# Kernel optimization log

Hardware: AMD Instinct MI355X
Metric: run time of the kernel (lower is better)

The kernel has to match this reference:

```python
import jax, jax.numpy as jnp
import numpy as np

BN_EPS = 1e-5


def setup_inputs() -> dict:
    key = jax.random.key(0)
    ks = jax.random.split(key, 6)
    B, C, N = 8, 256, 2048
    C4 = C // 4
    return {
        "x": jax.random.normal(ks[0], (B, C, N), dtype=jnp.float32),
        "wq": jax.random.normal(ks[1], (C4, C), dtype=jnp.float32) * (1.0 / np.sqrt(C)),
        "wv": jax.random.normal(ks[2], (C, C), dtype=jnp.float32) * (1.0 / np.sqrt(C)),
        "bv": jax.random.normal(ks[3], (C,), dtype=jnp.float32) * 0.02,
        "wt": jax.random.normal(ks[4], (C, C), dtype=jnp.float32) * (1.0 / np.sqrt(C)),
        "bt": jax.random.normal(ks[5], (C,), dtype=jnp.float32) * 0.02,
        "gamma": jnp.ones((C,), dtype=jnp.float32),
        "beta": jnp.zeros((C,), dtype=jnp.float32),
    }


def reference(x, wq, wv, bv, wt, bt, gamma, beta):
    # x: [B, C, N]. Conv1d(kernel=1) == per-point matmul.
    # q_conv and k_conv share the same weight in the original, so q == k.
    q = jnp.einsum('oc,bcn->bon', wq, x)            # [B, C/4, N]
    # ||q_i - q_j||_2 via the Gram identity (same math as norm of the diff tensor)
    sq = jnp.sum(q * q, axis=1)                     # [B, N]
    gram = jnp.einsum('bci,bcj->bij', q, q)         # [B, N, N]
    d2 = sq[:, :, None] - 2.0 * gram + sq[:, None, :]
    l2 = jnp.sqrt(jnp.maximum(d2, 0.0))             # [B, N, N]
    attn = jax.nn.softmax(-l2, axis=-1)             # rows = queries i
    v = jnp.einsum('oc,bcn->bon', wv, x) + bv[None, :, None]   # [B, C, N]
    # einsum('bij,bkj->bik') then permute(0,2,1) == contract j directly to [B, C, N]
    x_r = jnp.einsum('bij,bcj->bci', attn, v)       # [B, C, N]
    t = jnp.einsum('oc,bcn->bon', wt, x_r) + bt[None, :, None]
    # BatchNorm1d in training mode: batch stats over (B, N), biased variance
    mean = jnp.mean(t, axis=(0, 2), keepdims=True)
    var = jnp.mean((t - mean) ** 2, axis=(0, 2), keepdims=True)
    bn = gamma[None, :, None] * (t - mean) * jax.lax.rsqrt(var + BN_EPS) + beta[None, :, None]
    return x + jnp.maximum(bn, 0.0)
```

## Files before the change

kernel.cpp:

```cpp
#include <hip/hip_runtime.h>
#include <math.h>

#define BDIM 8
#define CDIM 256
#define C4DIM 64
#define NDIM 2048
#define LOG2E_SQ 2.0813689810056077f
#define NEG_2LOG2E_SQ -4.1627379620112154f

typedef short bf16x8 __attribute__((ext_vector_type(8)));
typedef float f32x4 __attribute__((ext_vector_type(4)));

__device__ inline unsigned cvt_pk(float lo, float hi) {
  unsigned r;
  asm("v_cvt_pk_bf16_f32 %0, %1, %2" : "=v"(r) : "v"(lo), "v"(hi));
  return r;
}
__device__ inline float bflo(unsigned u) {
  u <<= 16; float f; __builtin_memcpy(&f, &u, 4); return f;
}
__device__ inline float bfhi(unsigned u) {
  u &= 0xffff0000u; float f; __builtin_memcpy(&f, &u, 4); return f;
}

__global__ __launch_bounds__(256) void prep_kernel(const float* __restrict__ x,
                                                   const float* __restrict__ wq,
                                                   const float* __restrict__ wv,
                                                   const float* __restrict__ wt,
                                                   short* __restrict__ xT,
                                                   short* __restrict__ wqb,
                                                   short* __restrict__ wvb,
                                                   short* __restrict__ wtb,
                                                   float* __restrict__ bnsum) {
  __shared__ float tile[64][65];
  const int fb = blockIdx.x, t = threadIdx.x;
  if (fb < 1024) {
    const int b = fb >> 7, c0 = ((fb >> 5) & 3) * 64, n0 = (fb & 31) * 64;
    const int cl = t >> 2, ng = (t & 3) * 16;
#pragma unroll
    for (int kk = 0; kk < 4; ++kk) {
      float4 v = *(const float4*)&x[((size_t)(b * CDIM + c0 + cl)) * NDIM + n0 + ng + kk * 4];
      tile[cl][ng + kk * 4 + 0] = v.x; tile[cl][ng + kk * 4 + 1] = v.y;
      tile[cl][ng + kk * 4 + 2] = v.z; tile[cl][ng + kk * 4 + 3] = v.w;
    }
    __syncthreads();
    const int nl = t >> 2, cg = (t & 3) * 16;
    unsigned u[8];
#pragma unroll
    for (int e = 0; e < 8; ++e)
      u[e] = cvt_pk(tile[cg + 2 * e][nl], tile[cg + 2 * e + 1][nl]);
    short* dst = &xT[((size_t)b * NDIM + n0 + nl) * CDIM + c0 + cg];
    *(uint4*)&dst[0] = make_uint4(u[0], u[1], u[2], u[3]);
    *(uint4*)&dst[8] = make_uint4(u[4], u[5], u[6], u[7]);
  } else if (fb < 1168) {
    const int idx = ((fb - 1024) * 256 + t) * 4;
    const float* src; short* dst; int off;
    if (idx < 16384)      { src = wq; dst = wqb; off = idx; }
    else if (idx < 81920) { src = wv; dst = wvb; off = idx - 16384; }
    else                  { src = wt; dst = wtb; off = idx - 81920; }
    float4 v = *(const float4*)&src[off];
    *(uint2*)&dst[off] = make_uint2(cvt_pk(v.x, v.y), cvt_pk(v.z, v.w));
  } else {
    bnsum[t] = 0.f; bnsum[256 + t] = 0.f;
  }
}

template<bool STATS>
__device__ __forceinline__ void gemm128(const short* __restrict__ Wb,
                                        const short* __restrict__ Xt,
                                        const float* __restrict__ bias,
                                        short* __restrict__ OUT,
                                        float* __restrict__ bnsum,
                                        float* __restrict__ bnss,
                                        int b, int n0, int c0, int t) {
  const int w = t >> 6, l = t & 63, il = l & 15, g = l >> 4;
  const int wn = w & 1, wc = w >> 1;
  const size_t arow = (size_t)b * NDIM + n0 + wn * 64;
  const int ccol = c0 + wc * 64;
  f32x4 acc[4][4] = {};
#pragma unroll
  for (int ks = 0; ks < 8; ++ks) {
    const int k0 = ks * 32;
    bf16x8 af[4], bfr[4];
#pragma unroll
    for (int nt = 0; nt < 4; ++nt)
      af[nt] = *(const bf16x8*)&Xt[(arow + nt * 16 + il) * CDIM + k0 + g * 8];
#pragma unroll
    for (int ct = 0; ct < 4; ++ct)
      bfr[ct] = *(const bf16x8*)&Wb[(size_t)(ccol + ct * 16 + il) * CDIM + k0 + g * 8];
#pragma unroll
    for (int nt = 0; nt < 4; ++nt)
#pragma unroll
      for (int ct = 0; ct < 4; ++ct)
        acc[nt][ct] = __builtin_amdgcn_mfma_f32_16x16x32_bf16(af[nt], bfr[ct], acc[nt][ct], 0, 0, 0);
  }
#pragma unroll
  for (int ct = 0; ct < 4; ++ct) {
    const int c = ccol + ct * 16 + il;
    const float bs = bias[c];
    float s = 0.f, ss = 0.f;
#pragma unroll
    for (int nt = 0; nt < 4; ++nt) {
      const int n = n0 + wn * 64 + nt * 16 + g * 4;
      float y0 = acc[nt][ct][0] + bs, y1 = acc[nt][ct][1] + bs;
      float y2 = acc[nt][ct][2] + bs, y3 = acc[nt][ct][3] + bs;
      *(uint2*)&OUT[((size_t)(b * CDIM + c)) * NDIM + n] =
          make_uint2(cvt_pk(y0, y1), cvt_pk(y2, y3));
      if (STATS) {
        s += y0 + y1 + y2 + y3;
        ss += y0 * y0 + y1 * y1 + y2 * y2 + y3 * y3;
      }
    }
    if (STATS) {
      s += __shfl_xor(s, 16, 64);   s += __shfl_xor(s, 32, 64);
      ss += __shfl_xor(ss, 16, 64); ss += __shfl_xor(ss, 32, 64);
      if (l < 16) { atomicAdd(&bnsum[c], s); atomicAdd(&bnss[c], ss); }
    }
  }
}

__global__ __launch_bounds__(256) void qv_gemm(const short* __restrict__ wqb,
                                               const short* __restrict__ wvb,
                                               const short* __restrict__ xT,
                                               const float* __restrict__ bv,
                                               short* __restrict__ qT,
                                               float* __restrict__ sq2,
                                               short* __restrict__ vbf) {
  const int fb = blockIdx.x, t = threadIdx.x;
  if (fb < 256) {
    const int b = fb >> 5, c0 = ((fb >> 4) & 1) * 128, n0 = (fb & 15) * 128;
    gemm128<false>(wvb, xT, bv, vbf, nullptr, nullptr, b, n0, c0, t);
  } else {
    const int f = fb - 256;
    const int b = f >> 5, n0 = (f & 31) * 64;
    const int w = t >> 6, l = t & 63, il = l & 15, g = l >> 4;
    const int nw = n0 + w * 16;
    f32x4 acc[4] = {};
#pragma unroll
    for (int ks = 0; ks < 8; ++ks) {
      const int k0 = ks * 32;
      bf16x8 bx = *(const bf16x8*)&xT[((size_t)b * NDIM + nw + il) * CDIM + k0 + g * 8];
#pragma unroll
      for (int ot = 0; ot < 4; ++ot) {
        bf16x8 aw = *(const bf16x8*)&wqb[(size_t)(ot * 16 + il) * CDIM + k0 + g * 8];
        acc[ot] = __builtin_amdgcn_mfma_f32_16x16x32_bf16(aw, bx, acc[ot], 0, 0, 0);
      }
    }
    float sqs = 0.f;
#pragma unroll
    for (int ot = 0; ot < 4; ++ot) {
      unsigned u0 = cvt_pk(acc[ot][0], acc[ot][1]);
      unsigned u1 = cvt_pk(acc[ot][2], acc[ot][3]);
      *(uint2*)&qT[((size_t)b * NDIM + nw + il) * C4DIM + ot * 16 + g * 4] = make_uint2(u0, u1);
      float f0 = bflo(u0), f1 = bfhi(u0), f2 = bflo(u1), f3 = bfhi(u1);
      sqs += f0 * f0 + f1 * f1 + f2 * f2 + f3 * f3;
    }
    sqs += __shfl_xor(sqs, 16, 64);
    sqs += __shfl_xor(sqs, 32, 64);
    if (l < 16) sq2[(size_t)b * NDIM + nw + l] = sqs * LOG2E_SQ;
  }
}

__global__ __launch_bounds__(256) void attn_mfma(const short* __restrict__ qT,
                                                 const short* __restrict__ Vb16,
                                                 const float* __restrict__ sq2,
                                                 short* __restrict__ xrT) {
  __shared__ __align__(16) short vj[2][64 * 32];
  __shared__ __align__(16) short qj[2][32 * 64];
  __shared__ __align__(16) short wlds[4][16][40];

  const int bid = blockIdx.x;
  const int swz = (bid & 7) * 128 + (bid >> 3);
  const int i0 = (swz & 31) * 64;
  const int cq = (swz >> 5) & 3;
  const int b  = swz >> 7;

  const int t = threadIdx.x;
  const int w = t >> 6, l = t & 63, il = l & 15, g = l >> 4;

  const short* qTb = qT + (size_t)b * NDIM * C4DIM;
  const short* Vbb = Vb16 + ((size_t)b * CDIM + cq * 64) * NDIM;
  const float* sqb = sq2 + (size_t)b * NDIM;

  const int iglob = i0 + w * 16 + il;
  const bf16x8 bq0 = *(const bf16x8*)&qTb[(size_t)iglob * C4DIM + g * 8];
  const bf16x8 bq1 = *(const bf16x8*)&qTb[(size_t)iglob * C4DIM + 32 + g * 8];
  const float sqi = sqb[iglob];

  const int vcb = t >> 2, vs = t & 3;
  const int vd = vcb * 32 + ((vs ^ ((vcb >> 1) & 3)) << 3);
  const int qrow = t >> 3, qslot = t & 7;
  const int qd = qrow * 64 + ((qslot ^ (qrow & 7)) << 3);

  f32x4 acc[4];
#pragma unroll
  for (int k = 0; k < 4; ++k) acc[k] = {0.f, 0.f, 0.f, 0.f};
  float sumw = 0.f;

  f32x4 sqc0, sqc1;
  {
    bf16x8 vr0 = *(const bf16x8*)&Vbb[(size_t)vcb * NDIM + vs * 8];
    *(bf16x8*)&vj[0][vd] = vr0;
    bf16x8 qr = *(const bf16x8*)&qTb[(size_t)qrow * C4DIM + qslot * 8];
    *(bf16x8*)&qj[0][qd] = qr;
    sqc0 = *(const f32x4*)&sqb[g * 4];
    sqc1 = *(const f32x4*)&sqb[16 + g * 4];
  }
  __syncthreads();

  const int NT = NDIM / 32;
  for (int jt = 0; jt < NT; ++jt) {
    const int p = jt & 1;
    const bool hn = (jt + 1 < NT);
    const int j0n = jt * 32 + 32;

    bf16x8 vr0 = {}, qr = {};
    f32x4 sqn0 = {}, sqn1 = {};
    if (hn) {
      vr0 = *(const bf16x8*)&Vbb[(size_t)vcb * NDIM + j0n + vs * 8];
      qr  = *(const bf16x8*)&qTb[(size_t)(j0n + qrow) * C4DIM + qslot * 8];
      sqn0 = *(const f32x4*)&sqb[j0n + g * 4];
      sqn1 = *(const f32x4*)&sqb[j0n + 16 + g * 4];
    }

    const short* qbuf = &qj[p][0];
    const short* vbuf = &vj[p][0];

#pragma unroll
    for (int h = 0; h < 2; ++h) {
      const int row = h * 16 + il;
      bf16x8 aJ0 = *(const bf16x8*)&qbuf[row * 64 + ((g ^ (il & 7)) << 3)];
      bf16x8 aJ1 = *(const bf16x8*)&qbuf[row * 64 + (((4 + g) ^ (il & 7)) << 3)];
      f32x4 s = {0.f, 0.f, 0.f, 0.f};
      s = __builtin_amdgcn_mfma_f32_16x16x32_bf16(aJ0, bq0, s, 0, 0, 0);
      s = __builtin_amdgcn_mfma_f32_16x16x32_bf16(aJ1, bq1, s, 0, 0, 0);
      const f32x4 sqh = h ? sqc1 : sqc0;
      float wv[4];
#pragma unroll
      for (int r = 0; r < 4; ++r) {
        float e = fmaxf(fmaf(NEG_2LOG2E_SQ, s[r], sqi + sqh[r]), 0.f);
        wv[r] = __builtin_amdgcn_exp2f(-__builtin_amdgcn_sqrtf(e));
        sumw += wv[r];
      }
      *(uint2*)&wlds[w][il][h * 16 + g * 4] =
          make_uint2(cvt_pk(wv[0], wv[1]), cvt_pk(wv[2], wv[3]));
    }

    const bf16x8 bw = *(const bf16x8*)&wlds[w][il][g * 8];

    __builtin_amdgcn_s_setprio(1);
#pragma unroll
    for (int ctl = 0; ctl < 4; ++ctl) {
      const int lr = ctl * 16 + il;
      bf16x8 aV = *(const bf16x8*)&vbuf[lr * 32 + ((g ^ ((il >> 1) & 3)) << 3)];
      acc[ctl] = __builtin_amdgcn_mfma_f32_16x16x32_bf16(aV, bw, acc[ctl], 0, 0, 0);
    }
    __builtin_amdgcn_s_setprio(0);

    if (hn) {
      *(bf16x8*)&vj[p ^ 1][vd] = vr0;
      *(bf16x8*)&qj[p ^ 1][qd] = qr;
      sqc0 = sqn0; sqc1 = sqn1;
    }
    __syncthreads();
  }

  sumw += __shfl_xor(sumw, 16, 64);
  sumw += __shfl_xor(sumw, 32, 64);
  const float inv = 1.f / sumw;
#pragma unroll
  for (int ctl = 0; ctl < 4; ++ctl) {
    float y0 = acc[ctl][0] * inv, y1 = acc[ctl][1] * inv;
    float y2 = acc[ctl][2] * inv, y3 = acc[ctl][3] * inv;
    *(uint2*)&xrT[((size_t)b * NDIM + iglob) * CDIM + cq * 64 + ctl * 16 + g * 4] =
        make_uint2(cvt_pk(y0, y1), cvt_pk(y2, y3));
  }
}

__global__ __launch_bounds__(256) void t_gemm(const short* __restrict__ wtb,
                                              const short* __restrict__ xrT,
                                              const float* __restrict__ bt,
                                              short* __restrict__ tbf,
                                              float* __restrict__ bnsum,
                                              float* __restrict__ bnss) {
  gemm128<true>(wtb, xrT, bt, tbf, bnsum, bnss,
                blockIdx.z, blockIdx.x * 128, blockIdx.y * 128, threadIdx.x);
}

__global__ __launch_bounds__(256) void final_kernel(const float* __restrict__ x,
                                                    const short* __restrict__ tbf,
                                                    const float* __restrict__ bnsum,
                                                    const float* __restrict__ bnss,
                                                    const float* __restrict__ gamma,
                                                    const float* __restrict__ beta,
                                                    float* __restrict__ out) {
  const size_t idx = ((size_t)blockIdx.x * 256 + threadIdx.x) << 2;
  const int c = (int)((idx >> 11) & 255);
  const float cnt = (float)(BDIM * NDIM);
  const float mean = bnsum[c] / cnt;
  const float var = fmaxf(bnss[c] / cnt - mean * mean, 0.f);
  const float sc = gamma[c] * rsqrtf(var + 1e-5f);
  const float sh = beta[c] - mean * sc;
  float4 xv = *(const float4*)&x[idx];
  uint2 tu = *(const uint2*)&tbf[idx];
  const float t0 = bflo(tu.x), t1 = bfhi(tu.x), t2 = bflo(tu.y), t3 = bfhi(tu.y);
  float4 r;
  r.x = xv.x + fmaxf(t0 * sc + sh, 0.f);
  r.y = xv.y + fmaxf(t1 * sc + sh, 0.f);
  r.z = xv.z + fmaxf(t2 * sc + sh, 0.f);
  r.w = xv.w + fmaxf(t3 * sc + sh, 0.f);
  *(float4*)&out[idx] = r;
}

extern "C" void kernel_launch(void* const* d_in, const int* in_sizes, int n_in,
                              void* d_out, int out_size, void* d_ws, size_t ws_size,
                              hipStream_t stream) {
  const float* x     = (const float*)d_in[0];
  const float* wq    = (const float*)d_in[1];
  const float* wv    = (const float*)d_in[2];
  const float* bv    = (const float*)d_in[3];
  const float* wt    = (const float*)d_in[4];
  const float* bt    = (const float*)d_in[5];
  const float* gamma = (const float*)d_in[6];
  const float* beta  = (const float*)d_in[7];
  float* out = (float*)d_out;
  char* ws = (char*)d_ws;

  short* xbT   = (short*)(ws);
  short* wqb   = (short*)(ws + ((size_t)9  << 20));
  short* wvb   = (short*)(ws + ((size_t)9  << 20) + (256 << 10));
  short* wtb   = (short*)(ws + ((size_t)9  << 20) + (512 << 10));
  short* qT    = (short*)(ws + ((size_t)10 << 20));
  float* sq2   = (float*)(ws + ((size_t)12 << 20));
  short* vbf   = (short*)(ws + ((size_t)13 << 20));
  short* xrT   = (short*)(ws + ((size_t)22 << 20));
  short* tbf   = vbf;
  float* bnsum = (float*)(ws + ((size_t)31 << 20));
  float* bnss  = bnsum + 256;

  prep_kernel<<<dim3(1169), 256, 0, stream>>>(x, wq, wv, wt, xbT, wqb, wvb, wtb, bnsum);
  qv_gemm<<<dim3(512), 256, 0, stream>>>(wqb, wvb, xbT, bv, qT, sq2, vbf);
  attn_mfma<<<dim3(1024), 256, 0, stream>>>(qT, vbf, sq2, xrT);
  t_gemm<<<dim3(16, 2, 8), 256, 0, stream>>>(wtb, xrT, bt, tbf, bnsum, bnss);
  final_kernel<<<dim3(4096), 256, 0, stream>>>(x, tbf, bnsum, bnss, gamma, beta, out);
}
```

Measured before the change: 122.2 us.

## Retile attention blocks to cover 32 query rows by 128 channels

```diff
diff --git a/kernel.cpp b/kernel.cpp
--- a/kernel.cpp
+++ b/kernel.cpp
@@ -161,25 +161,25 @@
   }
 }
 
-__global__ __launch_bounds__(256) void attn_mfma(const short* __restrict__ qT,
+__global__ __launch_bounds__(128) void attn_mfma(const short* __restrict__ qT,
                                                  const short* __restrict__ Vb16,
                                                  const float* __restrict__ sq2,
                                                  short* __restrict__ xrT) {
-  __shared__ __align__(16) short vj[2][64 * 32];
+  __shared__ __align__(16) short vj[2][128 * 32];
   __shared__ __align__(16) short qj[2][32 * 64];
-  __shared__ __align__(16) short wlds[4][16][40];
+  __shared__ __align__(16) short wlds[2][16][40];
 
   const int bid = blockIdx.x;
   const int swz = (bid & 7) * 128 + (bid >> 3);
-  const int i0 = (swz & 31) * 64;
-  const int cq = (swz >> 5) & 3;
-  const int b  = swz >> 7;
+  const int i0    = (swz & 63) * 32;
+  const int chalf = (swz >> 6) & 1;
+  const int b     = swz >> 7;
 
   const int t = threadIdx.x;
   const int w = t >> 6, l = t & 63, il = l & 15, g = l >> 4;
 
   const short* qTb = qT + (size_t)b * NDIM * C4DIM;
-  const short* Vbb = Vb16 + ((size_t)b * CDIM + cq * 64) * NDIM;
+  const short* Vbb = Vb16 + ((size_t)b * CDIM + chalf * 128) * NDIM;
   const float* sqb = sq2 + (size_t)b * NDIM;
 
   const int iglob = i0 + w * 16 + il;
@@ -192,17 +192,22 @@
   const int qrow = t >> 3, qslot = t & 7;
   const int qd = qrow * 64 + ((qslot ^ (qrow & 7)) << 3);
 
-  f32x4 acc[4];
-#pragma unroll
-  for (int k = 0; k < 4; ++k) acc[k] = {0.f, 0.f, 0.f, 0.f};
+  f32x4 acc[8];
+#pragma unroll
+  for (int k = 0; k < 8; ++k) acc[k] = {0.f, 0.f, 0.f, 0.f};
   float sumw = 0.f;
 
   f32x4 sqc0, sqc1;
   {
-    bf16x8 vr0 = *(const bf16x8*)&Vbb[(size_t)vcb * NDIM + vs * 8];
-    *(bf16x8*)&vj[0][vd] = vr0;
-    bf16x8 qr = *(const bf16x8*)&qTb[(size_t)qrow * C4DIM + qslot * 8];
-    *(bf16x8*)&qj[0][qd] = qr;
+#pragma unroll
+    for (int k = 0; k < 4; ++k) {
+      bf16x8 vr = *(const bf16x8*)&Vbb[(size_t)(vcb + 32 * k) * NDIM + vs * 8];
+      *(bf16x8*)&vj[0][vd + k * 1024] = vr;
+    }
+    bf16x8 qa = *(const bf16x8*)&qTb[(size_t)qrow * C4DIM + qslot * 8];
+    bf16x8 qb = *(const bf16x8*)&qTb[(size_t)(qrow + 16) * C4DIM + qslot * 8];
+    *(bf16x8*)&qj[0][qd] = qa;
+    *(bf16x8*)&qj[0][qd + 1024] = qb;
     sqc0 = *(const f32x4*)&sqb[g * 4];
     sqc1 = *(const f32x4*)&sqb[16 + g * 4];
   }
@@ -214,11 +219,14 @@
     const bool hn = (jt + 1 < NT);
     const int j0n = jt * 32 + 32;
 
-    bf16x8 vr0 = {}, qr = {};
+    bf16x8 nv[4] = {}, nqa = {}, nqb = {};
     f32x4 sqn0 = {}, sqn1 = {};
     if (hn) {
-      vr0 = *(const bf16x8*)&Vbb[(size_t)vcb * NDIM + j0n + vs * 8];
-      qr  = *(const bf16x8*)&qTb[(size_t)(j0n + qrow) * C4DIM + qslot * 8];
+#pragma unroll
+      for (int k = 0; k < 4; ++k)
+        nv[k] = *(const bf16x8*)&Vbb[(size_t)(vcb + 32 * k) * NDIM + j0n + vs * 8];
+      nqa = *(const bf16x8*)&qTb[(size_t)(j0n + qrow) * C4DIM + qslot * 8];
+      nqb = *(const bf16x8*)&qTb[(size_t)(j0n + qrow + 16) * C4DIM + qslot * 8];
       sqn0 = *(const f32x4*)&sqb[j0n + g * 4];
       sqn1 = *(const f32x4*)&sqb[j0n + 16 + g * 4];
     }
@@ -250,7 +258,7 @@
 
     __builtin_amdgcn_s_setprio(1);
 #pragma unroll
-    for (int ctl = 0; ctl < 4; ++ctl) {
+    for (int ctl = 0; ctl < 8; ++ctl) {
       const int lr = ctl * 16 + il;
       bf16x8 aV = *(const bf16x8*)&vbuf[lr * 32 + ((g ^ ((il >> 1) & 3)) << 3)];
       acc[ctl] = __builtin_amdgcn_mfma_f32_16x16x32_bf16(aV, bw, acc[ctl], 0, 0, 0);
@@ -258,8 +266,10 @@
     __builtin_amdgcn_s_setprio(0);
 
     if (hn) {
-      *(bf16x8*)&vj[p ^ 1][vd] = vr0;
-      *(bf16x8*)&qj[p ^ 1][qd] = qr;
+#pragma unroll
+      for (int k = 0; k < 4; ++k) *(bf16x8*)&vj[p ^ 1][vd + k * 1024] = nv[k];
+      *(bf16x8*)&qj[p ^ 1][qd] = nqa;
+      *(bf16x8*)&qj[p ^ 1][qd + 1024] = nqb;
       sqc0 = sqn0; sqc1 = sqn1;
     }
     __syncthreads();
@@ -269,10 +279,10 @@
   sumw += __shfl_xor(sumw, 32, 64);
   const float inv = 1.f / sumw;
 #pragma unroll
-  for (int ctl = 0; ctl < 4; ++ctl) {
+  for (int ctl = 0; ctl < 8; ++ctl) {
     float y0 = acc[ctl][0] * inv, y1 = acc[ctl][1] * inv;
     float y2 = acc[ctl][2] * inv, y3 = acc[ctl][3] * inv;
-    *(uint2*)&xrT[((size_t)b * NDIM + iglob) * CDIM + cq * 64 + ctl * 16 + g * 4] =
+    *(uint2*)&xrT[((size_t)b * NDIM + iglob) * CDIM + chalf * 128 + ctl * 16 + g * 4] =
         make_uint2(cvt_pk(y0, y1), cvt_pk(y2, y3));
   }
 }
@@ -340,7 +350,7 @@
 
   prep_kernel<<<dim3(1169), 256, 0, stream>>>(x, wq, wv, wt, xbT, wqb, wvb, wtb, bnsum);
   qv_gemm<<<dim3(512), 256, 0, stream>>>(wqb, wvb, xbT, bv, qT, sq2, vbf);
-  attn_mfma<<<dim3(1024), 256, 0, stream>>>(qT, vbf, sq2, xrT);
+  attn_mfma<<<dim3(1024), 128, 0, stream>>>(qT, vbf, sq2, xrT);
   t_gemm<<<dim3(16, 2, 8), 256, 0, stream>>>(wtb, xrT, bt, tbf, bnsum, bnss);
   final_kernel<<<dim3(4096), 256, 0, stream>>>(x, tbf, bnsum, bnss, gamma, beta, out);
 }
```

After: 114.3 us. 1.07x faster.
